# Kernel tuning notes

Hardware: AMD Instinct MI355X
Metric: run time of the kernel (lower is better)

Reference implementation:

```python
import jax, jax.numpy as jnp
import numpy as np
import math

C_IN = 256
NUM_CLASSES = 80
NUM_CONVS = 3
GROUPS = 16
EPS = 1e-5
FEAT_SHAPES = [(2, C_IN, 100, 128), (2, C_IN, 50, 64), (2, C_IN, 25, 32), (2, C_IN, 13, 16), (2, C_IN, 7, 8)]


def conv2d(x, w, b):
    # x: [N,C,H,W], w: [O,I,3,3] -> SAME padding, stride 1
    y = jax.lax.conv_general_dilated(x, w, window_strides=(1, 1), padding='SAME',
                                     dimension_numbers=('NCHW', 'OIHW', 'NCHW'))
    return y + b[None, :, None, None]


def group_norm(x, gamma, beta):
    N, C, H, W = x.shape
    xr = x.reshape(N, GROUPS, C // GROUPS, H, W)
    m = xr.mean(axis=(2, 3, 4), keepdims=True)
    v = xr.var(axis=(2, 3, 4), keepdims=True)
    xn = ((xr - m) * jax.lax.rsqrt(v + EPS)).reshape(N, C, H, W)
    return xn * gamma[None, :, None, None] + beta[None, :, None, None]


def tower(x, ws, bs, gs, gbs):
    for i in range(NUM_CONVS):
        x = jax.nn.relu(group_norm(conv2d(x, ws[i], bs[i]), gs[i], gbs[i]))
    return x


def permut(x):
    # torch permutTensor: [N,C,H,W] -> [N, H*W, C]
    N, C, H, W = x.shape
    return x.transpose(0, 2, 3, 1).reshape(N, H * W, C)


def setup_inputs() -> dict:
    key = jax.random.key(0)
    ks = list(jax.random.split(key, 32))
    d = {}
    for i, shp in enumerate(FEAT_SHAPES):
        d[f'feat{i + 3}'] = jax.random.normal(ks[i], shp, dtype=jnp.float32)
    std = 0.01
    d['cls_conv_w'] = jax.random.normal(ks[5], (NUM_CONVS, C_IN, C_IN, 3, 3), dtype=jnp.float32) * std
    d['cls_conv_b'] = jnp.zeros((NUM_CONVS, C_IN), jnp.float32)
    d['cls_gn_g'] = jnp.ones((NUM_CONVS, C_IN), jnp.float32)
    d['cls_gn_b'] = jnp.zeros((NUM_CONVS, C_IN), jnp.float32)
    d['cls_logits_w'] = jax.random.normal(ks[6], (NUM_CLASSES, C_IN, 3, 3), dtype=jnp.float32) * std
    d['cls_logits_b'] = jnp.full((NUM_CLASSES,), -math.log((1 - 0.01) / 0.01), jnp.float32)
    d['reg_conv_w'] = jax.random.normal(ks[7], (NUM_CONVS, C_IN, C_IN, 3, 3), dtype=jnp.float32) * std
    d['reg_conv_b'] = jnp.zeros((NUM_CONVS, C_IN), jnp.float32)
    d['reg_gn_g'] = jnp.ones((NUM_CONVS, C_IN), jnp.float32)
    d['reg_gn_b'] = jnp.zeros((NUM_CONVS, C_IN), jnp.float32)
    d['bbox_reg_w'] = jax.random.normal(ks[8], (4, C_IN, 3, 3), dtype=jnp.float32) * std
    d['bbox_reg_b'] = jnp.zeros((4,), jnp.float32)
    d['ctr_w'] = jax.random.normal(ks[9], (1, C_IN, 3, 3), dtype=jnp.float32) * std
    d['ctr_b'] = jnp.zeros((1,), jnp.float32)
    return d


def reference(feat3, feat4, feat5, feat6, feat7,
              cls_conv_w, cls_conv_b, cls_gn_g, cls_gn_b, cls_logits_w, cls_logits_b,
              reg_conv_w, reg_conv_b, reg_gn_g, reg_gn_b,
              bbox_reg_w, bbox_reg_b, ctr_w, ctr_b):
    feats = [feat3, feat4, feat5, feat6, feat7]
    per_level = []
    for f in feats:
        # classification branch
        c = tower(f, cls_conv_w, cls_conv_b, cls_gn_g, cls_gn_b)
        cls = permut(conv2d(c, cls_logits_w, cls_logits_b))          # [N, HW, 80]
        r = tower(f, reg_conv_w, reg_conv_b, reg_gn_g, reg_gn_b)
        reg = permut(jax.nn.relu(conv2d(r, bbox_reg_w, bbox_reg_b)))  # [N, HW, 4]
        ctr = permut(conv2d(r, ctr_w, ctr_b))                         # [N, HW, 1]
        per_level.append(jnp.concatenate([cls, reg, ctr], axis=-1))
    # concat over pyramid levels -> [N, total_points, 85]
    return jnp.concatenate(per_level, axis=1)
```

## Files before the change

kernel.cpp:

```cpp
#include <hip/hip_runtime.h>

#define NCLS 80
#define TPOINTS 17064
#define GN_EPS 1e-5f

typedef float v4f __attribute__((ext_vector_type(4)));
typedef short v8s __attribute__((ext_vector_type(8)));

__device__ __forceinline__ unsigned short f2bf(float f) {
    unsigned u = __float_as_uint(f);
    unsigned r = (u + 0x7FFFu + ((u >> 16) & 1u)) >> 16;
    return (unsigned short)r;
}
__device__ __forceinline__ float bf2f(unsigned short h) {
    return __uint_as_float(((unsigned)h) << 16);
}
__device__ __forceinline__ void gload16(const unsigned short* g, unsigned short* l) {
    __builtin_amdgcn_global_load_lds(
        (const __attribute__((address_space(1))) unsigned int*)g,
        (__attribute__((address_space(3))) unsigned int*)l, 16, 0, 0);
}

struct Lv { int t_conv, t_gn, t_prep, t_h5, xo, P2W, PP, HW, W, H, lwW, loff; };
struct Tab { Lv lv[5]; };

template<int HEAD>
__global__ __launch_bounds__(256) void conv_k(
    const unsigned short* __restrict__ xin, size_t xin_brs,
    const unsigned short* __restrict__ wt, size_t wt_brs, int wrows,
    const float* __restrict__ bias_c, const float* __restrict__ bias_r,
    unsigned short* __restrict__ yout, float* __restrict__ stats, int layer,
    float* __restrict__ out, int CO, int co_out, int relu_cnt,
    Tab tb)
{
    __shared__ unsigned short sA[2 * 128 * 32];
    __shared__ unsigned short sB[2 * 128 * 32];
    const int tid = threadIdx.x, lane = tid & 63, wave = tid >> 6;
    const int bx = blockIdx.x, z = blockIdx.z;
    const int n = z & 1, br = z >> 1;
    int L = 0;
    while (L < 4 && bx >= tb.lv[L + 1].t_conv) ++L;
    const Lv lv = tb.lv[L];
    const int pp0 = (bx - lv.t_conv) * 128;
    const int co0 = HEAD ? 0 : blockIdx.y * 128;
    const size_t XELs = 9200640;

    v4f acc[4][4];
#pragma unroll
    for (int i = 0; i < 4; ++i)
#pragma unroll
        for (int j = 0; j < 4; ++j) acc[i][j] = (v4f)0.f;

    const unsigned short* wtb = wt + (size_t)br * wt_brs;
    const float* bias = br ? bias_r : bias_c;
    const unsigned short* xb = xin + (size_t)br * xin_brs +
                               (size_t)lv.xo + (size_t)n * lv.PP * 256;

    const int r0 = wave * 32;
    const int lr = lane >> 2;
    const int lc = ((lane & 3) ^ ((lane >> 3) & 3)) * 8;
    const unsigned short* ag = wtb + (size_t)(co0 + r0 + lr) * 256 + lc;
    const unsigned short* bg = xb + (size_t)(pp0 + r0 + lr) * 256 + lc;
    unsigned short* la = &sA[r0 * 32];
    unsigned short* lb = &sB[r0 * 32];
    const size_t wstride = (size_t)wrows * 256;

    const int col = lane & 15, q = lane >> 4;
    const int wco = (wave & 1) * 64, wpos = (wave >> 1) * 64;
    const int qs = (q ^ ((col >> 1) & 3)) << 3;
    int ard[4], brd[4];
#pragma unroll
    for (int i = 0; i < 4; ++i) {
        ard[i] = (wco  + i * 16 + col) * 32 + qs;
        brd[i] = (wpos + i * 16 + col) * 32 + qs;
    }

    auto addrs = [&](int step, const unsigned short*& at, const unsigned short*& bt) {
        const int t = step >> 3, kb = step & 7;
        const ptrdiff_t off = ((ptrdiff_t)(t / 3) - 1) * lv.P2W + (t % 3) - 1;
        at = ag + (size_t)t * wstride + kb * 32;
        bt = bg + off * 256 + kb * 32;
    };

    for (int pair = 0; pair < 36; ++pair) {
        const unsigned short *at0, *bt0, *at1, *bt1;
        addrs(2 * pair,     at0, bt0);
        addrs(2 * pair + 1, at1, bt1);
        __syncthreads();
        gload16(at0,            la);
        gload16(at0 + 16 * 256, la + 16 * 32);
        gload16(bt0,            lb);
        gload16(bt0 + 16 * 256, lb + 16 * 32);
        gload16(at1,            la + 4096);
        gload16(at1 + 16 * 256, la + 4096 + 16 * 32);
        gload16(bt1,            lb + 4096);
        gload16(bt1 + 16 * 256, lb + 4096 + 16 * 32);
        __syncthreads();
#pragma unroll
        for (int h = 0; h < 2; ++h) {
            const int hb = h * 4096;
            v8s af[4], bfr[4];
#pragma unroll
            for (int i = 0; i < 4; ++i) af[i]  = *(const v8s*)&sA[hb + ard[i]];
#pragma unroll
            for (int j = 0; j < 4; ++j) bfr[j] = *(const v8s*)&sB[hb + brd[j]];
#pragma unroll
            for (int i = 0; i < 4; ++i)
#pragma unroll
                for (int j = 0; j < 4; ++j)
                    acc[i][j] = __builtin_amdgcn_mfma_f32_16x16x32_bf16(
                        af[i], bfr[j], acc[i][j], 0, 0, 0);
        }
    }

    if (!HEAD) {
        unsigned short* yb = yout + (size_t)br * XELs + (size_t)lv.xo +
                             (size_t)n * lv.PP * 256;
        const int slot = br * 3 + layer;
#pragma unroll
        for (int i = 0; i < 4; ++i) {
            const int cobase = co0 + wco + i * 16 + q * 4;
            const float4 b4 = *(const float4*)(bias + cobase);
            float s = 0.f, ss = 0.f;
#pragma unroll
            for (int j = 0; j < 4; ++j) {
                const int pp = pp0 + wpos + j * 16 + col;
                const unsigned h2 = (unsigned)pp / (unsigned)lv.P2W;
                const unsigned w2 = (unsigned)pp - h2 * lv.P2W;
                const bool in = (h2 >= 1u) & (h2 <= (unsigned)lv.H) &
                                (w2 >= 1u) & (w2 <= (unsigned)lv.W);
                float v0 = acc[i][j][0] + b4.x;
                float v1 = acc[i][j][1] + b4.y;
                float v2 = acc[i][j][2] + b4.z;
                float v3 = acc[i][j][3] + b4.w;
                if (in) {
                    ushort4 pk;
                    pk.x = f2bf(v0); pk.y = f2bf(v1);
                    pk.z = f2bf(v2); pk.w = f2bf(v3);
                    *(ushort4*)(yb + (size_t)pp * 256 + cobase) = pk;
                    s  += v0 + v1 + v2 + v3;
                    ss += v0 * v0 + v1 * v1 + v2 * v2 + v3 * v3;
                }
            }
#pragma unroll
            for (int o = 32; o > 0; o >>= 1) {
                s  += __shfl_down(s, o, 64);
                ss += __shfl_down(ss, o, 64);
            }
            if (lane == 0) {
                const int g = cobase >> 4;
                const int si = (((slot * 5 + L) * 32) + n * 16 + g) * 2;
                atomicAdd(&stats[si + 0], s);
                atomicAdd(&stats[si + 1], ss);
            }
        }
    } else {
#pragma unroll
        for (int i = 0; i < 4; ++i) {
            const int cobase = wco + i * 16 + q * 4;
            float bv[4];
#pragma unroll
            for (int k = 0; k < 4; ++k)
                bv[k] = (cobase + k < CO) ? bias[cobase + k] : 0.f;
#pragma unroll
            for (int j = 0; j < 4; ++j) {
                const int pp = pp0 + wpos + j * 16 + col;
                const unsigned h2 = (unsigned)pp / (unsigned)lv.P2W;
                const unsigned w2 = (unsigned)pp - h2 * lv.P2W;
                const bool in = (h2 >= 1u) & (h2 <= (unsigned)lv.H) &
                                (w2 >= 1u) & (w2 <= (unsigned)lv.W);
                if (in) {
                    const int p = (h2 - 1) * lv.W + (w2 - 1);
                    float* ob = out + ((size_t)n * TPOINTS + lv.loff + p) * 85 + co_out;
#pragma unroll
                    for (int k = 0; k < 4; ++k) {
                        const int co = cobase + k;
                        if (co < CO) {
                            float v = acc[i][j][k] + bv[k];
                            if (co < relu_cnt) v = fmaxf(v, 0.f);
                            ob[co] = v;
                        }
                    }
                }
            }
        }
    }
}

__global__ __launch_bounds__(256) void head5_k(
    const unsigned short* __restrict__ xin,
    const unsigned short* __restrict__ wt,
    const float* __restrict__ bias, float* __restrict__ out, Tab tb)
{
    __shared__ unsigned short sA[16 * 32];
    __shared__ unsigned short sB[256 * 32];
    const int tid = threadIdx.x, lane = tid & 63, wave = tid >> 6;
    const int bx = blockIdx.x, n = blockIdx.z;
    int L = 0;
    while (L < 4 && bx >= tb.lv[L + 1].t_h5) ++L;
    const Lv lv = tb.lv[L];
    const int pp0 = (bx - lv.t_h5) * 256;

    v4f acc[4];
#pragma unroll
    for (int j = 0; j < 4; ++j) acc[j] = (v4f)0.f;

    const unsigned short* xb = xin + (size_t)lv.xo + (size_t)n * lv.PP * 256;
    const unsigned short* brow = xb + (size_t)(pp0 + tid) * 256;
    const int bs = (tid >> 1) & 3;
    int bw[4];
#pragma unroll
    for (int c = 0; c < 4; ++c) bw[c] = tid * 32 + ((c ^ bs) << 3);
    const unsigned short* arow = wt + (size_t)tid * 256;

    const int col = lane & 15, q = lane >> 4;
    const int qs = (q ^ ((col >> 1) & 3)) << 3;
    const int ard = col * 32 + qs;
    const int wb = wave * 64;
    int brd[4];
#pragma unroll
    for (int j = 0; j < 4; ++j) brd[j] = (wb + j * 16 + col) * 32 + qs;

    for (int step = 0; step < 72; ++step) {
        const int t = step >> 3, kb = step & 7;
        const ptrdiff_t off = ((ptrdiff_t)(t / 3) - 1) * lv.P2W + (t % 3) - 1;
        const unsigned short* bt = brow + off * 256 + kb * 32;
        uint4 bv[4];
#pragma unroll
        for (int c = 0; c < 4; ++c) bv[c] = *(const uint4*)(bt + c * 8);
        uint4 av[4];
        if (tid < 16) {
            const unsigned short* at = arow + (size_t)t * (16 * 256) + kb * 32;
#pragma unroll
            for (int c = 0; c < 4; ++c) av[c] = *(const uint4*)(at + c * 8);
        }
        __syncthreads();
#pragma unroll
        for (int c = 0; c < 4; ++c) *(uint4*)&sB[bw[c]] = bv[c];
        if (tid < 16) {
#pragma unroll
            for (int c = 0; c < 4; ++c) *(uint4*)&sA[bw[c]] = av[c];
        }
        __syncthreads();
        v8s af = *(const v8s*)&sA[ard];
        v8s bfr[4];
#pragma unroll
        for (int j = 0; j < 4; ++j) bfr[j] = *(const v8s*)&sB[brd[j]];
#pragma unroll
        for (int j = 0; j < 4; ++j)
            acc[j] = __builtin_amdgcn_mfma_f32_16x16x32_bf16(
                af, bfr[j], acc[j], 0, 0, 0);
    }

    float bv4[4];
#pragma unroll
    for (int k = 0; k < 4; ++k) {
        const int co = q * 4 + k;
        bv4[k] = (co < 5) ? bias[co] : 0.f;
    }
#pragma unroll
    for (int j = 0; j < 4; ++j) {
        const int pp = pp0 + wb + j * 16 + col;
        const unsigned h2 = (unsigned)pp / (unsigned)lv.P2W;
        const unsigned w2 = (unsigned)pp - h2 * lv.P2W;
        const bool in = (h2 >= 1u) & (h2 <= (unsigned)lv.H) &
                        (w2 >= 1u) & (w2 <= (unsigned)lv.W);
        if (in) {
            const int p = (h2 - 1) * lv.W + (w2 - 1);
            float* ob = out + ((size_t)n * TPOINTS + lv.loff + p) * 85 + 80;
#pragma unroll
            for (int k = 0; k < 4; ++k) {
                const int co = q * 4 + k;
                if (co < 5) {
                    float v = acc[j][k] + bv4[k];
                    if (co < 4) v = fmaxf(v, 0.f);
                    ob[co] = v;
                }
            }
        }
    }
}

__global__ __launch_bounds__(256) void gn_k(
    unsigned short* __restrict__ x, const float* __restrict__ stats, int layer,
    const float* __restrict__ g_c, const float* __restrict__ be_c,
    const float* __restrict__ g_r, const float* __restrict__ be_r, Tab tb)
{
    const int tid = threadIdx.x, bx = blockIdx.x, z = blockIdx.z;
    const int n = z & 1, br = z >> 1;
    const size_t XELs = 9200640;
    int L = 0;
    while (L < 4 && bx >= tb.lv[L + 1].t_gn) ++L;
    const Lv lv = tb.lv[L];
    const int pos = (bx - lv.t_gn) * 32 + (tid >> 3);
    if (pos >= lv.HW) return;
    const int slot = br * 3 + layer;
    const float* gamma = (br ? g_r : g_c) + layer * 256;
    const float* beta  = (br ? be_r : be_c) + layer * 256;
    const int c0 = (tid & 7) * 32;
    const int h = pos >> lv.lwW, w = pos & (lv.W - 1);
    const int pp = (h + 1) * lv.P2W + (w + 1);
    unsigned short* p = x + (size_t)br * XELs + (size_t)lv.xo +
                        ((size_t)n * lv.PP + pp) * 256 + c0;
    const float inv = 1.0f / (16.0f * (float)lv.HW);
    const int sb = ((slot * 5 + L) * 32 + n * 16) * 2;

    float scv[32], shv[32];
#pragma unroll
    for (int gg = 0; gg < 2; ++gg) {
        const int g = (c0 >> 4) + gg;
        const float m = stats[sb + g * 2 + 0] * inv;
        const float v = stats[sb + g * 2 + 1] * inv - m * m;
        const float rs = rsqrtf(v + GN_EPS);
#pragma unroll
        for (int k = 0; k < 16; ++k) {
            const int c = g * 16 + k;
            const float sc = rs * gamma[c];
            scv[gg * 16 + k] = sc;
            shv[gg * 16 + k] = beta[c] - m * sc;
        }
    }
#pragma unroll
    for (int u = 0; u < 4; ++u) {
        uint4 a = *(const uint4*)(p + u * 8);
        unsigned wds[4] = {a.x, a.y, a.z, a.w};
#pragma unroll
        for (int k = 0; k < 4; ++k) {
            const int e = u * 8 + k * 2;
            float lo = bf2f((unsigned short)(wds[k] & 0xffffu));
            float hi = bf2f((unsigned short)(wds[k] >> 16));
            lo = fmaxf(lo * scv[e]     + shv[e],     0.f);
            hi = fmaxf(hi * scv[e + 1] + shv[e + 1], 0.f);
            wds[k] = (unsigned)f2bf(lo) | ((unsigned)f2bf(hi) << 16);
        }
        uint4 o; o.x = wds[0]; o.y = wds[1]; o.z = wds[2]; o.w = wds[3];
        *(uint4*)(p + u * 8) = o;
    }
}

__global__ __launch_bounds__(256) void prepx_k(
    const float* f0, const float* f1, const float* f2, const float* f3,
    const float* f4, unsigned short* __restrict__ xo, Tab tb)
{
    const float* fs[5] = {f0, f1, f2, f3, f4};
    const int tid = threadIdx.x, bx = blockIdx.x, n = blockIdx.z;
    int L = 0;
    while (L < 4 && bx >= tb.lv[L + 1].t_prep) ++L;
    const Lv lv = tb.lv[L];
    const int pos = (bx - lv.t_prep) * 64 + (tid & 63);
    const int wave = tid >> 6;
    if (pos >= lv.HW) return;
    const int h = pos >> lv.lwW, w = pos & (lv.W - 1);
    const int pp = (h + 1) * lv.P2W + (w + 1);
    const float* src = fs[L] + (size_t)n * 256 * lv.HW + pos;
    unsigned short* dst = xo + (size_t)lv.xo + ((size_t)n * lv.PP + pp) * 256;
#pragma unroll
    for (int k = 0; k < 16; ++k) {
        const int c = wave * 64 + k * 4;
        ushort4 pk;
        pk.x = f2bf(src[(size_t)(c + 0) * lv.HW]);
        pk.y = f2bf(src[(size_t)(c + 1) * lv.HW]);
        pk.z = f2bf(src[(size_t)(c + 2) * lv.HW]);
        pk.w = f2bf(src[(size_t)(c + 3) * lv.HW]);
        *(ushort4*)(dst + c) = pk;
    }
}

__global__ __launch_bounds__(256) void prepwt_k(
    const float* __restrict__ cw, const float* __restrict__ rw,
    unsigned short* __restrict__ dst)
{
    const int idx = blockIdx.x * 256 + threadIdx.x;
    const int ci = idx & 255, co = (idx >> 8) & 255, r = idx >> 16;
    const int tap = r % 9, layer = (r / 9) % 3, br = r / 27;
    const float* s = br ? rw : cw;
    dst[(size_t)r * 65536 + co * 256 + ci] =
        f2bf(s[(((size_t)layer * 256 + co) * 256 + ci) * 9 + tap]);
}

__global__ __launch_bounds__(256) void prepwh_k(
    const float* __restrict__ src, unsigned short* __restrict__ dst,
    int CO, int rows, int roff)
{
    const int idx = blockIdx.x * 256 + threadIdx.x;
    if (idx >= CO * 2304) return;
    const int ci = idx & 255, rr = idx >> 8;
    const int tap = rr % 9, co = rr / 9;
    dst[((size_t)tap * rows + roff + co) * 256 + ci] =
        f2bf(src[((size_t)co * 256 + ci) * 9 + tap]);
}

extern "C" void kernel_launch(void* const* d_in, const int* in_sizes, int n_in,
                              void* d_out, int out_size, void* d_ws, size_t ws_size,
                              hipStream_t stream) {
    const float* f0 = (const float*)d_in[0];
    const float* f1 = (const float*)d_in[1];
    const float* f2 = (const float*)d_in[2];
    const float* f3 = (const float*)d_in[3];
    const float* f4 = (const float*)d_in[4];
    const float* cls_w  = (const float*)d_in[5];
    const float* cls_b  = (const float*)d_in[6];
    const float* cls_g  = (const float*)d_in[7];
    const float* cls_be = (const float*)d_in[8];
    const float* log_w  = (const float*)d_in[9];
    const float* log_b  = (const float*)d_in[10];
    const float* reg_w  = (const float*)d_in[11];
    const float* reg_b  = (const float*)d_in[12];
    const float* reg_g  = (const float*)d_in[13];
    const float* reg_be = (const float*)d_in[14];
    const float* bbox_w = (const float*)d_in[15];
    const float* bbox_b = (const float*)d_in[16];
    const float* ctr_w  = (const float*)d_in[17];
    const float* ctr_b  = (const float*)d_in[18];
    float* out = (float*)d_out;

    Tab tb;
    tb.lv[0] = {   0,    0,    0,    0,   0,       130, 13260, 12800, 128, 100, 7, 0     };
    tb.lv[1] = { 104,  400,  200,  52,  6789120,    66,  3432,  3200,  64,  50, 6, 12800 };
    tb.lv[2] = { 131,  500,  250,  66,  8546304,    34,   918,   800,  32,  25, 5, 16000 };
    tb.lv[3] = { 139,  525,  263,  70,  9016320,    18,   270,   208,  16,  13, 4, 16800 };
    tb.lv[4] = { 142,  532,  267,  72,  9154560,    10,    90,    56,   8,   7, 3, 17008 };
    const int NT_CONV = 143, NT_GN = 534, NT_PREP = 268, NT_H5 = 73;
    const size_t XEL = 9200640;

    char* base = (char*)d_ws;
    size_t o = 0;
    auto take = [&](size_t bytes) {
        char* p = base + o; o += (bytes + 255) & ~(size_t)255; return p;
    };
    take(131072);
    unsigned short* PX = (unsigned short*)take(XEL * 2);
    take(131072);
    unsigned short* B1 = (unsigned short*)take(XEL * 2 * 2);
    take(131072);
    unsigned short* B2 = (unsigned short*)take(XEL * 2 * 2);
    take(131072);
    unsigned short* WT  = (unsigned short*)take((size_t)54 * 65536 * 2);
    unsigned short* WHC = (unsigned short*)take((size_t)9 * 128 * 256 * 2);
    unsigned short* WHR = (unsigned short*)take((size_t)9 * 16 * 256 * 2);
    float* ST  = (float*)take(1920 * 4);
    float* RB5 = (float*)take(32);

    hipMemsetAsync(PX, 0, XEL * 2, stream);
    hipMemsetAsync(B1, 0, XEL * 4, stream);
    hipMemsetAsync(B2, 0, XEL * 4, stream);
    hipMemsetAsync(ST, 0, 1920 * 4, stream);
    hipMemcpyAsync(RB5,     bbox_b, 4 * 4, hipMemcpyDeviceToDevice, stream);
    hipMemcpyAsync(RB5 + 4, ctr_b,  1 * 4, hipMemcpyDeviceToDevice, stream);

    prepwt_k<<<dim3(13824), dim3(256), 0, stream>>>(cls_w, reg_w, WT);
    prepwh_k<<<dim3(720), dim3(256), 0, stream>>>(log_w,  WHC, 80, 128, 0);
    prepwh_k<<<dim3(36),  dim3(256), 0, stream>>>(bbox_w, WHR, 4, 16, 0);
    prepwh_k<<<dim3(9),   dim3(256), 0, stream>>>(ctr_w,  WHR, 1, 16, 4);

    const dim3 blk(256);
    prepx_k<<<dim3(NT_PREP, 1, 2), blk, 0, stream>>>(f0, f1, f2, f3, f4, PX, tb);

    const size_t WBRS = (size_t)27 * 65536;
    unsigned short* cin[3]  = {PX, B1, B2};
    size_t          cbrs[3] = {0, XEL, XEL};
    unsigned short* cout_[3] = {B1, B2, B1};
    for (int i = 0; i < 3; ++i) {
        conv_k<0><<<dim3(NT_CONV, 2, 4), blk, 0, stream>>>(
            cin[i], cbrs[i], WT + (size_t)i * 9 * 65536, WBRS, 256,
            cls_b + i * 256, reg_b + i * 256,
            cout_[i], ST, i, nullptr, 0, 0, 0, tb);
        gn_k<<<dim3(NT_GN, 1, 4), blk, 0, stream>>>(
            cout_[i], ST, i, cls_g, cls_be, reg_g, reg_be, tb);
    }
    conv_k<1><<<dim3(NT_CONV, 1, 2), blk, 0, stream>>>(
        B1, 0, WHC, 0, 128, log_b, log_b,
        nullptr, nullptr, 0, out, NCLS, 0, 0, tb);
    head5_k<<<dim3(NT_H5, 1, 2), blk, 0, stream>>>(
        B1 + XEL, WHR, RB5, out, tb);
}
```

Baseline: 1.058 ms.

## Double-buffer LDS tiles to overlap global loads with MFMA compute

Doubles the shared-memory A/B buffers and restructures the K loop so the next pair of K-steps is loaded into the alternate buffer while MFMAs run on the current one. This removes the load-then-wait serialization and halves the barriers per pair. It doubles LDS use per block (to 64KB), which may reduce occupancy, and it relies on barrier placement for correctness.

Result: slower. 1.209 ms (+14.3%).

```diff
diff --git a/kernel.cpp b/kernel.cpp
--- a/kernel.cpp
+++ b/kernel.cpp
@@ -33,8 +33,8 @@
     float* __restrict__ out, int CO, int co_out, int relu_cnt,
     Tab tb)
 {
-    __shared__ unsigned short sA[2 * 128 * 32];
-    __shared__ unsigned short sB[2 * 128 * 32];
+    __shared__ unsigned short sA[2 * 2 * 128 * 32];
+    __shared__ unsigned short sB[2 * 2 * 128 * 32];
     const int tid = threadIdx.x, lane = tid & 63, wave = tid >> 6;
     const int bx = blockIdx.x, z = blockIdx.z;
     const int n = z & 1, br = z >> 1;
@@ -82,23 +82,24 @@
         bt = bg + off * 256 + kb * 32;
     };
 
-    for (int pair = 0; pair < 36; ++pair) {
+    auto stage = [&](int pair, int bsel) {
         const unsigned short *at0, *bt0, *at1, *bt1;
         addrs(2 * pair,     at0, bt0);
         addrs(2 * pair + 1, at1, bt1);
-        __syncthreads();
-        gload16(at0,            la);
-        gload16(at0 + 16 * 256, la + 16 * 32);
-        gload16(bt0,            lb);
-        gload16(bt0 + 16 * 256, lb + 16 * 32);
-        gload16(at1,            la + 4096);
-        gload16(at1 + 16 * 256, la + 4096 + 16 * 32);
-        gload16(bt1,            lb + 4096);
-        gload16(bt1 + 16 * 256, lb + 4096 + 16 * 32);
-        __syncthreads();
+        gload16(at0,            la + bsel);
+        gload16(at0 + 16 * 256, la + bsel + 16 * 32);
+        gload16(bt0,            lb + bsel);
+        gload16(bt0 + 16 * 256, lb + bsel + 16 * 32);
+        gload16(at1,            la + bsel + 4096);
+        gload16(at1 + 16 * 256, la + bsel + 4096 + 16 * 32);
+        gload16(bt1,            lb + bsel + 4096);
+        gload16(bt1 + 16 * 256, lb + bsel + 4096 + 16 * 32);
+    };
+
+    auto compute = [&](int bsel) {
 #pragma unroll
         for (int h = 0; h < 2; ++h) {
-            const int hb = h * 4096;
+            const int hb = bsel + h * 4096;
             v8s af[4], bfr[4];
 #pragma unroll
             for (int i = 0; i < 4; ++i) af[i]  = *(const v8s*)&sA[hb + ard[i]];
@@ -111,6 +112,20 @@
                     acc[i][j] = __builtin_amdgcn_mfma_f32_16x16x32_bf16(
                         af[i], bfr[j], acc[i][j], 0, 0, 0);
         }
+    };
+
+    stage(0, 0);
+    __syncthreads();
+#pragma unroll 1
+    for (int p = 0; p < 36; p += 2) {
+        stage(p + 1, 8192);
+        __builtin_amdgcn_sched_barrier(0);
+        compute(0);
+        __syncthreads();
+        if (p + 2 < 36) stage(p + 2, 0);
+        __builtin_amdgcn_sched_barrier(0);
+        compute(8192);
+        __syncthreads();
     }
 
     if (!HEAD) {
```

## Triple-buffer LDS tiles so async global-to-LDS loads overlap MFMA compute

Applied to the files above, without the earlier changes.

The conv main loop used to load two K-steps into LDS and then wait on a full barrier before computing, so loads and MFMA work alternated. It now keeps three LDS buffers and issues the async global_load_lds for step s+2 before computing step s. An explicit vmcnt wait makes sure only the needed step has landed, which hides global memory latency behind matrix math. The cost is 50% more LDS per block, which may lower occupancy, plus hand-written waitcnt and barrier logic that has to stay correct.

Result: slower. 1.124 ms (+6.3%).

```diff
diff --git a/kernel.cpp b/kernel.cpp
--- a/kernel.cpp
+++ b/kernel.cpp
@@ -33,8 +33,8 @@
     float* __restrict__ out, int CO, int co_out, int relu_cnt,
     Tab tb)
 {
-    __shared__ unsigned short sA[2 * 128 * 32];
-    __shared__ unsigned short sB[2 * 128 * 32];
+    __shared__ unsigned short sA[3 * 128 * 32];
+    __shared__ unsigned short sB[3 * 128 * 32];
     const int tid = threadIdx.x, lane = tid & 63, wave = tid >> 6;
     const int bx = blockIdx.x, z = blockIdx.z;
     const int n = z & 1, br = z >> 1;
@@ -75,43 +75,56 @@
         brd[i] = (wpos + i * 16 + col) * 32 + qs;
     }
 
-    auto addrs = [&](int step, const unsigned short*& at, const unsigned short*& bt) {
+    auto stage = [&](int step, int off) {
         const int t = step >> 3, kb = step & 7;
-        const ptrdiff_t off = ((ptrdiff_t)(t / 3) - 1) * lv.P2W + (t % 3) - 1;
-        at = ag + (size_t)t * wstride + kb * 32;
-        bt = bg + off * 256 + kb * 32;
+        const ptrdiff_t goff = ((ptrdiff_t)(t / 3) - 1) * lv.P2W + (t % 3) - 1;
+        const unsigned short* at = ag + (size_t)t * wstride + kb * 32;
+        const unsigned short* bt = bg + goff * 256 + kb * 32;
+        gload16(at,            la + off);
+        gload16(at + 16 * 256, la + off + 16 * 32);
+        gload16(bt,            lb + off);
+        gload16(bt + 16 * 256, lb + off + 16 * 32);
     };
 
-    for (int pair = 0; pair < 36; ++pair) {
-        const unsigned short *at0, *bt0, *at1, *bt1;
-        addrs(2 * pair,     at0, bt0);
-        addrs(2 * pair + 1, at1, bt1);
-        __syncthreads();
-        gload16(at0,            la);
-        gload16(at0 + 16 * 256, la + 16 * 32);
-        gload16(bt0,            lb);
-        gload16(bt0 + 16 * 256, lb + 16 * 32);
-        gload16(at1,            la + 4096);
-        gload16(at1 + 16 * 256, la + 4096 + 16 * 32);
-        gload16(bt1,            lb + 4096);
-        gload16(bt1 + 16 * 256, lb + 4096 + 16 * 32);
-        __syncthreads();
-#pragma unroll
-        for (int h = 0; h < 2; ++h) {
-            const int hb = h * 4096;
-            v8s af[4], bfr[4];
-#pragma unroll
-            for (int i = 0; i < 4; ++i) af[i]  = *(const v8s*)&sA[hb + ard[i]];
-#pragma unroll
-            for (int j = 0; j < 4; ++j) bfr[j] = *(const v8s*)&sB[hb + brd[j]];
-#pragma unroll
-            for (int i = 0; i < 4; ++i)
-#pragma unroll
-                for (int j = 0; j < 4; ++j)
-                    acc[i][j] = __builtin_amdgcn_mfma_f32_16x16x32_bf16(
-                        af[i], bfr[j], acc[i][j], 0, 0, 0);
-        }
-    }
+    auto compute = [&](int off) {
+        v8s af[4], bfr[4];
+#pragma unroll
+        for (int i = 0; i < 4; ++i) af[i]  = *(const v8s*)&sA[off + ard[i]];
+#pragma unroll
+        for (int j = 0; j < 4; ++j) bfr[j] = *(const v8s*)&sB[off + brd[j]];
+#pragma unroll
+        for (int i = 0; i < 4; ++i)
+#pragma unroll
+            for (int j = 0; j < 4; ++j)
+                acc[i][j] = __builtin_amdgcn_mfma_f32_16x16x32_bf16(
+                    af[i], bfr[j], acc[i][j], 0, 0, 0);
+    };
+
+    stage(0, 0);
+    stage(1, 4096);
+    int cur = 0, nx = 4096, fut = 8192;
+#pragma unroll 1
+    for (int s = 0; s < 70; ++s) {
+        stage(s + 2, fut);
+        __builtin_amdgcn_sched_barrier(0);
+        asm volatile("s_waitcnt vmcnt(8)" ::: "memory");
+        __builtin_amdgcn_s_barrier();
+        __builtin_amdgcn_sched_barrier(0);
+        compute(cur);
+        __builtin_amdgcn_sched_barrier(0);
+        __builtin_amdgcn_s_barrier();
+        const int t = cur; cur = nx; nx = fut; fut = t;
+    }
+    asm volatile("s_waitcnt vmcnt(4)" ::: "memory");
+    __builtin_amdgcn_s_barrier();
+    __builtin_amdgcn_sched_barrier(0);
+    compute(cur);
+    __builtin_amdgcn_sched_barrier(0);
+    __builtin_amdgcn_s_barrier();
+    asm volatile("s_waitcnt vmcnt(0)" ::: "memory");
+    __builtin_amdgcn_s_barrier();
+    __builtin_amdgcn_sched_barrier(0);
+    compute(nx);
 
     if (!HEAD) {
         unsigned short* yb = yout + (size_t)br * XELs + (size_t)lv.xo +
```
